# Kernel tuning notes

Hardware: AMD Instinct MI355X
Metric: run time of the kernel (lower is better)

Reference implementation:

```python
import jax, jax.numpy as jnp
import numpy as np

N = 8192      # n_nodes
F = 512       # input feature dim
MLP = 512     # mlp_channels
C = 256       # output channels
H = 2         # MLP layers
KPI = 10      # power iterations
ALPHA = 0.1   # teleport probability


def setup_inputs() -> dict:
    key = jax.random.key(0)
    ks = jax.random.split(key, 10)
    features = jax.random.normal(ks[0], (N, F), dtype=jnp.float32)
    # dense normalized-adjacency surrogate: nonnegative, rows ~ sum to 1
    fltr = jax.random.uniform(ks[1], (N, N), dtype=jnp.float32) * (2.0 / N)
    s = 1.0 / np.sqrt(F)
    W_mlp0 = jax.random.normal(ks[2], (F, MLP), dtype=jnp.float32) * s
    b_mlp0 = jnp.zeros((MLP,), dtype=jnp.float32)
    W_mlp1 = jax.random.normal(ks[3], (MLP, MLP), dtype=jnp.float32) * (1.0 / np.sqrt(MLP))
    b_mlp1 = jnp.zeros((MLP,), dtype=jnp.float32)
    W_out = jax.random.normal(ks[4], (MLP, C), dtype=jnp.float32) * (1.0 / np.sqrt(MLP))
    b_out = jnp.zeros((C,), dtype=jnp.float32)
    return {"features": features, "fltr": fltr,
            "W_mlp0": W_mlp0, "b_mlp0": b_mlp0,
            "W_mlp1": W_mlp1, "b_mlp1": b_mlp1,
            "W_out": W_out, "b_out": b_out}


def reference(features, fltr, W_mlp0, b_mlp0, W_mlp1, b_mlp1, W_out, b_out):
    # MLP stage: per layer -> X = relu( A @ (X W + b) )   (dropout_rate = 0)
    x = features
    for W, b in ((W_mlp0, b_mlp0), (W_mlp1, b_mlp1)):
        x = jnp.matmul(fltr, jnp.matmul(x, W) + b)  # [N, MLP]
        x = jax.nn.relu(x)
    # output projection
    z0 = jnp.matmul(x, W_out) + b_out  # [N, C]
    # K-step APPNP power iteration: Z <- (1-alpha) A Z + alpha Z0
    def step(z, _):
        z = (1.0 - ALPHA) * jnp.matmul(fltr, z) + ALPHA * z0
        return z, None
    z, _ = jax.lax.scan(step, z0, None, length=KPI)
    return jax.nn.softmax(z, axis=-1)
```

## Files before the change

kernel.cpp:

```cpp
#include <hip/hip_runtime.h>

typedef unsigned short u16;
typedef __attribute__((ext_vector_type(8))) short bf16x8;
typedef __attribute__((ext_vector_type(4))) float f32x4;

__device__ __forceinline__ float bf2f(u16 u) {
    union { unsigned i; float f; } v; v.i = ((unsigned)u) << 16; return v.f;
}
__device__ __forceinline__ u16 f2bf(float f) {
    union { float f; unsigned i; } v; v.f = f;
    unsigned r = v.i + 0x7FFFu + ((v.i >> 16) & 1u);
    return (u16)(r >> 16);
}

#define GL2LDS(g, l) __builtin_amdgcn_global_load_lds(                         \
    (const __attribute__((address_space(1))) void*)(g),                        \
    (__attribute__((address_space(3))) void*)(l), 16, 0, 0)

template<int EPI, int AFP32>
__global__ __launch_bounds__(256, 4)
void gemm_bt(const void* __restrict__ Ap, int lda,
             const u16* __restrict__ Bt, int ldb,
             int KB,
             void* __restrict__ outp,
             const void* __restrict__ aux,
             int ldout, int NC)
{
    __shared__ u16 aL[128 * 64];
    __shared__ u16 bL[128 * 64];

    const int t = threadIdx.x;
    const int wid = t >> 6, lane = t & 63;
    const int quad = lane >> 4, l15 = lane & 15, l7 = lane & 7;
    const int m0 = blockIdx.x * 128, n0 = blockIdx.y * 128;
    const int sk = blockIdx.z;
    const int k0 = sk * KB * 64;

    f32x4 acc[4][4];
    const f32x4 z4 = {0.f, 0.f, 0.f, 0.f};
#pragma unroll
    for (int i = 0; i < 4; ++i)
#pragma unroll
        for (int j = 0; j < 4; ++j) acc[i][j] = z4;

    const int wm = (wid >> 1) * 64, wn = (wid & 1) * 64;

    if (AFP32 == 0) {
        const char* pa[4]; const char* pb[4]; int lo[4];
#pragma unroll
        for (int i = 0; i < 4; ++i) {
            int flat = i * 4096 + wid * 1024 + lane * 16;
            int row  = flat >> 7;
            int csrc = ((flat >> 4) & 7) ^ (row & 7);
            pa[i] = (const char*)Ap + ((size_t)(m0 + row) * lda + k0) * 2 + csrc * 16;
            pb[i] = (const char*)Bt + ((size_t)(n0 + row) * ldb + k0) * 2 + csrc * 16;
            lo[i] = i * 4096 + wid * 1024;
        }
        for (int kb = 0; kb < KB; ++kb) {
#pragma unroll
            for (int i = 0; i < 4; ++i) GL2LDS(pa[i], (char*)aL + lo[i]);
#pragma unroll
            for (int i = 0; i < 4; ++i) GL2LDS(pb[i], (char*)bL + lo[i]);
#pragma unroll
            for (int i = 0; i < 4; ++i) { pa[i] += 128; pb[i] += 128; }
            __syncthreads();
#pragma unroll
            for (int ks = 0; ks < 2; ++ks) {
                const int cr = ((ks * 4 + quad) ^ l7) * 8;
                bf16x8 av[4], bv[4];
#pragma unroll
                for (int mi = 0; mi < 4; ++mi)
                    av[mi] = *(const bf16x8*)(aL + (wm + mi * 16 + l15) * 64 + cr);
#pragma unroll
                for (int ni = 0; ni < 4; ++ni)
                    bv[ni] = *(const bf16x8*)(bL + (wn + ni * 16 + l15) * 64 + cr);
#pragma unroll
                for (int mi = 0; mi < 4; ++mi)
#pragma unroll
                    for (int ni = 0; ni < 4; ++ni)
                        acc[mi][ni] = __builtin_amdgcn_mfma_f32_16x16x32_bf16(
                            av[mi], bv[ni], acc[mi][ni], 0, 0, 0);
            }
            __syncthreads();
        }
    } else {
        for (int kb = 0; kb < KB; ++kb) {
            const int kbase = k0 + kb * 64;
#pragma unroll
            for (int i = 0; i < 4; ++i) {
                int flat = i * 4096 + t * 16;
                int row  = flat >> 7;
                int col  = (flat & 127) >> 1;
                bf16x8 v = *(const bf16x8*)(Bt + (size_t)(n0 + row) * ldb + kbase + col);
                *(bf16x8*)(bL + row * 64 + col) = v;
            }
            const float* Af = (const float*)Ap;
#pragma unroll
            for (int j = 0; j < 8; ++j) {
                int f = j * 256 + t;
                int r = f >> 4, c = (f & 15) * 4;
                float4 v = *(const float4*)(Af + (size_t)(m0 + r) * lda + kbase + c);
                ushort4 o;
                o.x = f2bf(v.x); o.y = f2bf(v.y);
                o.z = f2bf(v.z); o.w = f2bf(v.w);
                *(ushort4*)(aL + r * 64 + c) = o;
            }
            __syncthreads();
#pragma unroll
            for (int ks = 0; ks < 2; ++ks) {
                const int cr = (ks * 4 + quad) * 8;
                bf16x8 av[4], bv[4];
#pragma unroll
                for (int mi = 0; mi < 4; ++mi)
                    av[mi] = *(const bf16x8*)(aL + (wm + mi * 16 + l15) * 64 + cr);
#pragma unroll
                for (int ni = 0; ni < 4; ++ni)
                    bv[ni] = *(const bf16x8*)(bL + (wn + ni * 16 + l15) * 64 + cr);
#pragma unroll
                for (int mi = 0; mi < 4; ++mi)
#pragma unroll
                    for (int ni = 0; ni < 4; ++ni)
                        acc[mi][ni] = __builtin_amdgcn_mfma_f32_16x16x32_bf16(
                            av[mi], bv[ni], acc[mi][ni], 0, 0, 0);
            }
            __syncthreads();
        }
    }

    if (EPI == 0) {
#pragma unroll
        for (int ni = 0; ni < 4; ++ni) {
            int n = n0 + wn + ni * 16 + l15;
            float bvv = ((const float*)aux)[n];
            u16* ob = (u16*)outp + (size_t)n * ldout;
#pragma unroll
            for (int mi = 0; mi < 4; ++mi) {
                int m = m0 + wm + mi * 16 + quad * 4;
                ushort4 o;
                o.x = f2bf(acc[mi][ni][0] + bvv);
                o.y = f2bf(acc[mi][ni][1] + bvv);
                o.z = f2bf(acc[mi][ni][2] + bvv);
                o.w = f2bf(acc[mi][ni][3] + bvv);
                *(ushort4*)(ob + m) = o;
            }
        }
    } else if (EPI == 2) {
#pragma unroll
        for (int ni = 0; ni < 4; ++ni) {
            int n = n0 + wn + ni * 16 + l15;
            float* ob = (float*)outp + ((size_t)(sk * NC + n)) * 8192;
#pragma unroll
            for (int mi = 0; mi < 4; ++mi) {
                int m = m0 + wm + mi * 16 + quad * 4;
                float4 o;
                o.x = acc[mi][ni][0]; o.y = acc[mi][ni][1];
                o.z = acc[mi][ni][2]; o.w = acc[mi][ni][3];
                *(float4*)(ob + m) = o;
            }
        }
    } else if (EPI == 3) {
#pragma unroll
        for (int ni = 0; ni < 4; ++ni) {
            int n = n0 + wn + ni * 16 + l15;
            const u16* zrow = (const u16*)aux + (size_t)n * 8192;
            u16* ob = (u16*)outp + (size_t)n * ldout;
#pragma unroll
            for (int mi = 0; mi < 4; ++mi) {
                int m = m0 + wm + mi * 16 + quad * 4;
                ushort4 z0 = *(const ushort4*)(zrow + m);
                ushort4 o;
                o.x = f2bf(0.9f * acc[mi][ni][0] + 0.1f * bf2f(z0.x));
                o.y = f2bf(0.9f * acc[mi][ni][1] + 0.1f * bf2f(z0.y));
                o.z = f2bf(0.9f * acc[mi][ni][2] + 0.1f * bf2f(z0.z));
                o.w = f2bf(0.9f * acc[mi][ni][3] + 0.1f * bf2f(z0.w));
                *(ushort4*)(ob + m) = o;
            }
        }
    } else {
        u16* ob = (u16*)outp;
#pragma unroll
        for (int mi = 0; mi < 4; ++mi) {
            int m = m0 + wm + mi * 16 + quad * 4;
#pragma unroll
            for (int ni = 0; ni < 4; ++ni) {
                int n = n0 + wn + ni * 16 + l15;
#pragma unroll
                for (int r = 0; r < 4; ++r)
                    ob[(size_t)(m + r) * ldout + n] = f2bf(fmaxf(acc[mi][ni][r], 0.0f));
            }
        }
    }
}

__global__ __launch_bounds__(256)
void cvt_f2b_k(const float* __restrict__ in, u16* __restrict__ out, long n4)
{
    long i = (long)blockIdx.x * 256 + threadIdx.x;
    long stride = (long)gridDim.x * 256;
    for (; i < n4; i += stride) {
        float4 v = ((const float4*)in)[i];
        ushort4 o;
        o.x = f2bf(v.x); o.y = f2bf(v.y); o.z = f2bf(v.z); o.w = f2bf(v.w);
        ((ushort4*)out)[i] = o;
    }
}

__global__ __launch_bounds__(256)
void transpose_cvt_k(const float* __restrict__ in, u16* __restrict__ out,
                     int R, int C)
{
    __shared__ u16 tile[32][33];
    int tx = threadIdx.x, ty = threadIdx.y;
    int x = blockIdx.x * 32 + tx;
    int y0 = blockIdx.y * 32 + ty;
#pragma unroll
    for (int j = 0; j < 32; j += 8)
        tile[ty + j][tx] = f2bf(in[(size_t)(y0 + j) * C + x]);
    __syncthreads();
    int x2 = blockIdx.y * 32 + tx;
    int y2 = blockIdx.x * 32 + ty;
#pragma unroll
    for (int j = 0; j < 32; j += 8)
        out[(size_t)(y2 + j) * R + x2] = tile[tx][ty + j];
}

template<int S>
__global__ __launch_bounds__(256)
void combine_bias_k(const float* __restrict__ part, const float* __restrict__ bias,
                    u16* __restrict__ out, long NROW)
{
    const size_t Sz = (size_t)NROW * 8192;
    size_t e = ((size_t)blockIdx.x * 256 + threadIdx.x) * 4;
    int n = (int)(e >> 13);
    float b = bias[n];
    float4 s = *(const float4*)(part + e);
#pragma unroll
    for (int i = 1; i < S; ++i) {
        float4 v = *(const float4*)(part + (size_t)i * Sz + e);
        s.x += v.x; s.y += v.y; s.z += v.z; s.w += v.w;
    }
    ushort4 o;
    o.x = f2bf(s.x + b); o.y = f2bf(s.y + b);
    o.z = f2bf(s.z + b); o.w = f2bf(s.w + b);
    *(ushort4*)(out + e) = o;
}

template<int S>
__global__ __launch_bounds__(256)
void combine_mlp_k(const float* __restrict__ part, u16* __restrict__ y)
{
    __shared__ u16 L[64][68];
    const int t = threadIdx.x;
    const int mb = blockIdx.x * 64;
    const int nb = blockIdx.y * 64;
    const size_t Sz = (size_t)512 * 8192;
#pragma unroll
    for (int i = 0; i < 4; ++i) {
        int flat = i * 256 + t;
        int nl = flat >> 4;
        int mq = flat & 15;
        const float* p0 = part + (size_t)(nb + nl) * 8192 + mb + mq * 4;
        float4 a = *(const float4*)p0;
#pragma unroll
        for (int s = 1; s < S; ++s) {
            float4 v = *(const float4*)(p0 + (size_t)s * Sz);
            a.x += v.x; a.y += v.y; a.z += v.z; a.w += v.w;
        }
        ushort4 o;
        o.x = f2bf(fmaxf(a.x, 0.f)); o.y = f2bf(fmaxf(a.y, 0.f));
        o.z = f2bf(fmaxf(a.z, 0.f)); o.w = f2bf(fmaxf(a.w, 0.f));
        *(ushort4*)&L[nl][mq * 4] = o;
    }
    __syncthreads();
#pragma unroll
    for (int i = 0; i < 4; ++i) {
        int flat = i * 256 + t;
        int ml  = flat >> 4;
        int nl4 = (flat & 15) * 4;
        ushort4 o;
        o.x = L[nl4 + 0][ml]; o.y = L[nl4 + 1][ml];
        o.z = L[nl4 + 2][ml]; o.w = L[nl4 + 3][ml];
        *(ushort4*)(y + (size_t)(mb + ml) * 512 + nb + nl4) = o;
    }
}

template<int S>
__global__ __launch_bounds__(256)
void combine_iter_k(const float* __restrict__ part, const u16* __restrict__ z0T,
                    u16* __restrict__ zT)
{
    const size_t Sz = (size_t)256 * 8192;
    size_t e = ((size_t)blockIdx.x * 256 + threadIdx.x) * 4;
    float4 a = *(const float4*)(part + e);
#pragma unroll
    for (int s = 1; s < S; ++s) {
        float4 v = *(const float4*)(part + (size_t)s * Sz + e);
        a.x += v.x; a.y += v.y; a.z += v.z; a.w += v.w;
    }
    ushort4 z0 = *(const ushort4*)(z0T + e);
    ushort4 o;
    o.x = f2bf(0.9f * a.x + 0.1f * bf2f(z0.x));
    o.y = f2bf(0.9f * a.y + 0.1f * bf2f(z0.y));
    o.z = f2bf(0.9f * a.z + 0.1f * bf2f(z0.z));
    o.w = f2bf(0.9f * a.w + 0.1f * bf2f(z0.w));
    *(ushort4*)(zT + e) = o;
}

__global__ __launch_bounds__(256)
void softmax_k(const u16* __restrict__ zT, float* __restrict__ out)
{
    __shared__ u16 L[64][260];
    const int t = threadIdx.x;
    const int m0 = blockIdx.x * 64;
    const int tx = t & 15, ty = t >> 4;
#pragma unroll
    for (int i = 0; i < 16; ++i) {
        int n = i * 16 + ty;
        ushort4 v = *(const ushort4*)(zT + (size_t)n * 8192 + m0 + tx * 4);
        L[tx * 4 + 0][n] = v.x; L[tx * 4 + 1][n] = v.y;
        L[tx * 4 + 2][n] = v.z; L[tx * 4 + 3][n] = v.w;
    }
    __syncthreads();
    const int wid = t >> 6, lane = t & 63;
    for (int r = 0; r < 16; ++r) {
        int mm = wid * 16 + r;
        ushort4 u = *(const ushort4*)(&L[mm][lane * 4]);
        float f0 = bf2f(u.x), f1 = bf2f(u.y), f2 = bf2f(u.z), f3 = bf2f(u.w);
        float mx = fmaxf(fmaxf(f0, f1), fmaxf(f2, f3));
#pragma unroll
        for (int off = 32; off > 0; off >>= 1) mx = fmaxf(mx, __shfl_xor(mx, off));
        float e0 = __expf(f0 - mx), e1 = __expf(f1 - mx);
        float e2 = __expf(f2 - mx), e3 = __expf(f3 - mx);
        float s = e0 + e1 + e2 + e3;
#pragma unroll
        for (int off = 32; off > 0; off >>= 1) s += __shfl_xor(s, off);
        float inv = 1.0f / s;
        float4 o;
        o.x = e0 * inv; o.y = e1 * inv; o.z = e2 * inv; o.w = e3 * inv;
        *(float4*)(out + (size_t)(m0 + mm) * 256 + lane * 4) = o;
    }
}

extern "C" void kernel_launch(void* const* d_in, const int* in_sizes, int n_in,
                              void* d_out, int out_size, void* d_ws, size_t ws_size,
                              hipStream_t stream)
{
    const float* features = (const float*)d_in[0];
    const float* fltr     = (const float*)d_in[1];
    const float* W0       = (const float*)d_in[2];
    const float* b0       = (const float*)d_in[3];
    const float* W1       = (const float*)d_in[4];
    const float* b1       = (const float*)d_in[5];
    const float* Wo       = (const float*)d_in[6];
    const float* bo       = (const float*)d_in[7];

    dim3 tb(32, 8);

    char* p = (char*)d_ws;
    u16* fB  = (u16*)p;  p += (size_t)8192 * 512 * 2;
    u16* W0T = (u16*)p;  p += (size_t)512 * 512 * 2;
    u16* W1T = (u16*)p;  p += (size_t)512 * 512 * 2;
    u16* WoT = (u16*)p;  p += (size_t)256 * 512 * 2;
    u16* z0T = (u16*)p;  p += (size_t)256 * 8192 * 2;
    u16* zA  = (u16*)p;  p += (size_t)256 * 8192 * 2;
    u16* zB  = (u16*)p;  p += (size_t)256 * 8192 * 2;
    u16* tT  = (u16*)p;  p += (size_t)512 * 8192 * 2;
    u16* y   = (u16*)p;  p += (size_t)8192 * 512 * 2;
    float* part = (float*)p; p += (size_t)4 * 512 * 8192 * 4;
    size_t base_need = (size_t)(p - (char*)d_ws);
    u16* fltrB = (u16*)p;
    size_t full_need = base_need + (size_t)8192 * 8192 * 2;

    if (ws_size >= full_need) {
        cvt_f2b_k<<<2048, 256, 0, stream>>>(fltr, fltrB, (long)8192 * 8192 / 4);
        cvt_f2b_k<<<512, 256, 0, stream>>>(features, fB, (long)8192 * 512 / 4);
        transpose_cvt_k<<<dim3(16, 16), tb, 0, stream>>>(W0, W0T, 512, 512);
        transpose_cvt_k<<<dim3(16, 16), tb, 0, stream>>>(W1, W1T, 512, 512);
        transpose_cvt_k<<<dim3(8, 16),  tb, 0, stream>>>(Wo, WoT, 512, 256);

        gemm_bt<0, 0><<<dim3(64, 4, 1), 256, 0, stream>>>(fB, 512, W0T, 512, 8,
                                                          tT, b0, 8192, 0);
        gemm_bt<2, 0><<<dim3(64, 4, 2), 256, 0, stream>>>(fltrB, 8192, tT, 8192,
                                                          64, part, nullptr, 0, 512);
        combine_mlp_k<2><<<dim3(128, 8), 256, 0, stream>>>(part, y);
        gemm_bt<0, 0><<<dim3(64, 4, 1), 256, 0, stream>>>(y, 512, W1T, 512, 8,
                                                          tT, b1, 8192, 0);
        gemm_bt<2, 0><<<dim3(64, 4, 2), 256, 0, stream>>>(fltrB, 8192, tT, 8192,
                                                          64, part, nullptr, 0, 512);
        combine_mlp_k<2><<<dim3(128, 8), 256, 0, stream>>>(part, y);
        gemm_bt<0, 0><<<dim3(64, 2, 1), 256, 0, stream>>>(y, 512, WoT, 512, 8,
                                                          z0T, bo, 8192, 0);
        const u16* src = z0T;
        for (int it = 0; it < 10; ++it) {
            u16* dst = (it & 1) ? zB : zA;
            gemm_bt<2, 0><<<dim3(64, 2, 4), 256, 0, stream>>>(fltrB, 8192, src,
                                                              8192, 32, part,
                                                              nullptr, 0, 256);
            combine_iter_k<4><<<2048, 256, 0, stream>>>(part, z0T, dst);
            src = dst;
        }
        softmax_k<<<128, 256, 0, stream>>>(src, (float*)d_out);
    } else if (ws_size >= base_need) {
        cvt_f2b_k<<<512, 256, 0, stream>>>(features, fB, (long)8192 * 512 / 4);
        transpose_cvt_k<<<dim3(16, 16), tb, 0, stream>>>(W0, W0T, 512, 512);
        transpose_cvt_k<<<dim3(16, 16), tb, 0, stream>>>(W1, W1T, 512, 512);
        transpose_cvt_k<<<dim3(8, 16),  tb, 0, stream>>>(Wo, WoT, 512, 256);

        gemm_bt<2, 0><<<dim3(64, 4, 2), 256, 0, stream>>>(fB, 512, W0T, 512, 4,
                                                          part, nullptr, 0, 512);
        combine_bias_k<2><<<4096, 256, 0, stream>>>(part, b0, tT, 512);
        gemm_bt<2, 1><<<dim3(64, 4, 4), 256, 0, stream>>>(fltr, 8192, tT, 8192,
                                                          32, part, nullptr, 0, 512);
        combine_mlp_k<4><<<dim3(128, 8), 256, 0, stream>>>(part, y);
        gemm_bt<2, 0><<<dim3(64, 4, 2), 256, 0, stream>>>(y, 512, W1T, 512, 4,
                                                          part, nullptr, 0, 512);
        combine_bias_k<2><<<4096, 256, 0, stream>>>(part, b1, tT, 512);
        gemm_bt<2, 1><<<dim3(64, 4, 4), 256, 0, stream>>>(fltr, 8192, tT, 8192,
                                                          32, part, nullptr, 0, 512);
        combine_mlp_k<4><<<dim3(128, 8), 256, 0, stream>>>(part, y);
        gemm_bt<2, 0><<<dim3(64, 2, 4), 256, 0, stream>>>(y, 512, WoT, 512, 2,
                                                          part, nullptr, 0, 256);
        combine_bias_k<4><<<2048, 256, 0, stream>>>(part, bo, z0T, 256);
        const u16* src = z0T;
        for (int it = 0; it < 10; ++it) {
            u16* dst = (it & 1) ? zB : zA;
            gemm_bt<2, 1><<<dim3(64, 2, 8), 256, 0, stream>>>(fltr, 8192, src,
                                                              8192, 16, part,
                                                              nullptr, 0, 256);
            combine_iter_k<8><<<2048, 256, 0, stream>>>(part, z0T, dst);
            src = dst;
        }
        softmax_k<<<128, 256, 0, stream>>>(src, (float*)d_out);
    } else {
        char* w = (char*)d_ws;
        u16* fW0T = (u16*)w;  w += (size_t)512 * 512 * 2;
        u16* fW1T = (u16*)w;  w += (size_t)512 * 512 * 2;
        u16* fWoT = (u16*)w;  w += (size_t)256 * 512 * 2;
        u16* fz0T = (u16*)w;  w += (size_t)256 * 8192 * 2;
        char* rb = w;
        u16* ftT = (u16*)rb;
        u16* fy  = (u16*)(rb + (size_t)512 * 8192 * 2);
        u16* fzA = (u16*)rb;
        u16* fzB = (u16*)(rb + (size_t)256 * 8192 * 2);

        transpose_cvt_k<<<dim3(16, 16), tb, 0, stream>>>(W0, fW0T, 512, 512);
        transpose_cvt_k<<<dim3(16, 16), tb, 0, stream>>>(W1, fW1T, 512, 512);
        transpose_cvt_k<<<dim3(8, 16),  tb, 0, stream>>>(Wo, fWoT, 512, 256);
        gemm_bt<0, 1><<<dim3(64, 4), 256, 0, stream>>>(features, 512, fW0T, 512, 8,
                                                       ftT, b0, 8192, 0);
        gemm_bt<1, 1><<<dim3(64, 4), 256, 0, stream>>>(fltr, 8192, ftT, 8192, 128,
                                                       fy, nullptr, 512, 0);
        gemm_bt<0, 0><<<dim3(64, 4), 256, 0, stream>>>(fy, 512, fW1T, 512, 8,
                                                       ftT, b1, 8192, 0);
        gemm_bt<1, 1><<<dim3(64, 4), 256, 0, stream>>>(fltr, 8192, ftT, 8192, 128,
                                                       fy, nullptr, 512, 0);
        gemm_bt<0, 0><<<dim3(64, 2), 256, 0, stream>>>(fy, 512, fWoT, 512, 8,
                                                       fz0T, bo, 8192, 0);
        const u16* src = fz0T;
        for (int it = 0; it < 10; ++it) {
            u16* dst = (it & 1) ? fzB : fzA;
            gemm_bt<3, 1><<<dim3(64, 2), 256, 0, stream>>>(fltr, 8192, src, 8192,
                                                           128, dst, fz0T, 8192, 0);
            src = dst;
        }
        softmax_k<<<128, 256, 0, stream>>>(src, (float*)d_out);
    }
}
```

Measured before the change: 1.142 ms.

## Fuse split-K reduction into power-iteration GEMM via atomic last-block combine

Replaces the separate combine_iter_k launch after each split-K power-iteration GEMM with an in-kernel reduction. Each split writes its fp32 partials, bumps an atomic tile counter, and the last-arriving block sums the other splits' partials and applies the APPNP update epilogue. This removes ten extra kernel launches and the full partial re-read pass. The cost is a fence, an atomic per tile and serialized epilogue work in one block per tile. Correctness relies on the counter being zeroed once and using modulo across iterations.

```diff
diff --git a/kernel.cpp b/kernel.cpp
--- a/kernel.cpp
+++ b/kernel.cpp
@@ -17,17 +17,20 @@
     (const __attribute__((address_space(1))) void*)(g),                        \
     (__attribute__((address_space(3))) void*)(l), 16, 0, 0)
 
-template<int EPI, int AFP32>
+template<int EPI, int AFP32, int SK>
 __global__ __launch_bounds__(256, 4)
 void gemm_bt(const void* __restrict__ Ap, int lda,
              const u16* __restrict__ Bt, int ldb,
              int KB,
              void* __restrict__ outp,
              const void* __restrict__ aux,
-             int ldout, int NC)
+             int ldout, int NC,
+             float* __restrict__ part,
+             unsigned* __restrict__ ctr)
 {
     __shared__ u16 aL[128 * 64];
     __shared__ u16 bL[128 * 64];
+    __shared__ int lastFlag;
 
     const int t = threadIdx.x;
     const int wid = t >> 6, lane = t & 63;
@@ -176,6 +179,55 @@
                 *(ushort4*)(ob + m) = o;
             }
         }
+    } else if (EPI == 4) {
+#pragma unroll
+        for (int ni = 0; ni < 4; ++ni) {
+            int n = n0 + wn + ni * 16 + l15;
+            float* ob = part + ((size_t)(sk * NC + n)) * 8192;
+#pragma unroll
+            for (int mi = 0; mi < 4; ++mi) {
+                int m = m0 + wm + mi * 16 + quad * 4;
+                float4 o;
+                o.x = acc[mi][ni][0]; o.y = acc[mi][ni][1];
+                o.z = acc[mi][ni][2]; o.w = acc[mi][ni][3];
+                *(float4*)(ob + m) = o;
+            }
+        }
+        __threadfence();
+        if (t == 0) {
+            unsigned old = atomicAdd(&ctr[blockIdx.x * gridDim.y + blockIdx.y], 1u);
+            lastFlag = (((old + 1) % (unsigned)SK) == 0u) ? 1 : 0;
+        }
+        __syncthreads();
+        if (lastFlag) {
+            __threadfence();
+#pragma unroll
+            for (int ni = 0; ni < 4; ++ni) {
+                int n = n0 + wn + ni * 16 + l15;
+                const u16* zrow = (const u16*)aux + (size_t)n * 8192;
+                u16* ob = (u16*)outp + (size_t)n * ldout;
+#pragma unroll
+                for (int mi = 0; mi < 4; ++mi) {
+                    int m = m0 + wm + mi * 16 + quad * 4;
+                    float sx = acc[mi][ni][0], sy = acc[mi][ni][1];
+                    float sz = acc[mi][ni][2], sw = acc[mi][ni][3];
+#pragma unroll
+                    for (int s = 0; s < SK; ++s) {
+                        if (s == sk) continue;
+                        float4 v = *(const float4*)(part +
+                                     ((size_t)(s * NC + n)) * 8192 + m);
+                        sx += v.x; sy += v.y; sz += v.z; sw += v.w;
+                    }
+                    ushort4 z0 = *(const ushort4*)(zrow + m);
+                    ushort4 o;
+                    o.x = f2bf(0.9f * sx + 0.1f * bf2f(z0.x));
+                    o.y = f2bf(0.9f * sy + 0.1f * bf2f(z0.y));
+                    o.z = f2bf(0.9f * sz + 0.1f * bf2f(z0.z));
+                    o.w = f2bf(0.9f * sw + 0.1f * bf2f(z0.w));
+                    *(ushort4*)(ob + m) = o;
+                }
+            }
+        }
     } else {
         u16* ob = (u16*)outp;
 #pragma unroll
@@ -190,6 +242,13 @@
             }
         }
     }
+}
+
+__global__ __launch_bounds__(256)
+void zero_ctr_k(unsigned* __restrict__ c, int n)
+{
+    int i = blockIdx.x * 256 + threadIdx.x;
+    if (i < n) c[i] = 0u;
 }
 
 __global__ __launch_bounds__(256)
@@ -367,6 +426,7 @@
     u16* tT  = (u16*)p;  p += (size_t)512 * 8192 * 2;
     u16* y   = (u16*)p;  p += (size_t)8192 * 512 * 2;
     float* part = (float*)p; p += (size_t)4 * 512 * 8192 * 4;
+    unsigned* ctr = (unsigned*)p; p += 1024;
     size_t base_need = (size_t)(p - (char*)d_ws);
     u16* fltrB = (u16*)p;
     size_t full_need = base_need + (size_t)8192 * 8192 * 2;
@@ -377,26 +437,32 @@
         transpose_cvt_k<<<dim3(16, 16), tb, 0, stream>>>(W0, W0T, 512, 512);
         transpose_cvt_k<<<dim3(16, 16), tb, 0, stream>>>(W1, W1T, 512, 512);
         transpose_cvt_k<<<dim3(8, 16),  tb, 0, stream>>>(Wo, WoT, 512, 256);
-
-        gemm_bt<0, 0><<<dim3(64, 4, 1), 256, 0, stream>>>(fB, 512, W0T, 512, 8,
-                                                          tT, b0, 8192, 0);
-        gemm_bt<2, 0><<<dim3(64, 4, 2), 256, 0, stream>>>(fltrB, 8192, tT, 8192,
-                                                          64, part, nullptr, 0, 512);
+        zero_ctr_k<<<1, 256, 0, stream>>>(ctr, 256);
+
+        gemm_bt<0, 0, 1><<<dim3(64, 4, 1), 256, 0, stream>>>(fB, 512, W0T, 512, 8,
+                                                          tT, b0, 8192, 0,
+                                                          nullptr, nullptr);
+        gemm_bt<2, 0, 1><<<dim3(64, 4, 2), 256, 0, stream>>>(fltrB, 8192, tT, 8192,
+                                                          64, part, nullptr, 0, 512,
+                                                          nullptr, nullptr);
         combine_mlp_k<2><<<dim3(128, 8), 256, 0, stream>>>(part, y);
-        gemm_bt<0, 0><<<dim3(64, 4, 1), 256, 0, stream>>>(y, 512, W1T, 512, 8,
-                                                          tT, b1, 8192, 0);
-        gemm_bt<2, 0><<<dim3(64, 4, 2), 256, 0, stream>>>(fltrB, 8192, tT, 8192,
-                                                          64, part, nullptr, 0, 512);
+        gemm_bt<0, 0, 1><<<dim3(64, 4, 1), 256, 0, stream>>>(y, 512, W1T, 512, 8,
+                                                          tT, b1, 8192, 0,
+                                                          nullptr, nullptr);
+        gemm_bt<2, 0, 1><<<dim3(64, 4, 2), 256, 0, stream>>>(fltrB, 8192, tT, 8192,
+                                                          64, part, nullptr, 0, 512,
+                                                          nullptr, nullptr);
         combine_mlp_k<2><<<dim3(128, 8), 256, 0, stream>>>(part, y);
-        gemm_bt<0, 0><<<dim3(64, 2, 1), 256, 0, stream>>>(y, 512, WoT, 512, 8,
-                                                          z0T, bo, 8192, 0);
+        gemm_bt<0, 0, 1><<<dim3(64, 2, 1), 256, 0, stream>>>(y, 512, WoT, 512, 8,
+                                                          z0T, bo, 8192, 0,
+                                                          nullptr, nullptr);
         const u16* src = z0T;
         for (int it = 0; it < 10; ++it) {
             u16* dst = (it & 1) ? zB : zA;
-            gemm_bt<2, 0><<<dim3(64, 2, 4), 256, 0, stream>>>(fltrB, 8192, src,
-                                                              8192, 32, part,
-                                                              nullptr, 0, 256);
-            combine_iter_k<4><<<2048, 256, 0, stream>>>(part, z0T, dst);
+            gemm_bt<4, 0, 4><<<dim3(64, 2, 4), 256, 0, stream>>>(fltrB, 8192, src,
+                                                              8192, 32, dst,
+                                                              z0T, 8192, 256,
+                                                              part, ctr);
             src = dst;
         }
         softmax_k<<<128, 256, 0, stream>>>(src, (float*)d_out);
@@ -406,27 +472,33 @@
         transpose_cvt_k<<<dim3(16, 16), tb, 0, stream>>>(W1, W1T, 512, 512);
         transpose_cvt_k<<<dim3(8, 16),  tb, 0, stream>>>(Wo, WoT, 512, 256);
 
-        gemm_bt<2, 0><<<dim3(64, 4, 2), 256, 0, stream>>>(fB, 512, W0T, 512, 4,
-                                                          part, nullptr, 0, 512);
+        gemm_bt<2, 0, 1><<<dim3(64, 4, 2), 256, 0, stream>>>(fB, 512, W0T, 512, 4,
+                                                          part, nullptr, 0, 512,
+                                                          nullptr, nullptr);
         combine_bias_k<2><<<4096, 256, 0, stream>>>(part, b0, tT, 512);
-        gemm_bt<2, 1><<<dim3(64, 4, 4), 256, 0, stream>>>(fltr, 8192, tT, 8192,
-                                                          32, part, nullptr, 0, 512);
+        gemm_bt<2, 1, 1><<<dim3(64, 4, 4), 256, 0, stream>>>(fltr, 8192, tT, 8192,
+                                                          32, part, nullptr, 0, 512,
+                                                          nullptr, nullptr);
         combine_mlp_k<4><<<dim3(128, 8), 256, 0, stream>>>(part, y);
-        gemm_bt<2, 0><<<dim3(64, 4, 2), 256, 0, stream>>>(y, 512, W1T, 512, 4,
-                                                          part, nullptr, 0, 512);
+        gemm_bt<2, 0, 1><<<dim3(64, 4, 2), 256, 0, stream>>>(y, 512, W1T, 512, 4,
+                                                          part, nullptr, 0, 512,
+                                                          nullptr, nullptr);
         combine_bias_k<2><<<4096, 256, 0, stream>>>(part, b1, tT, 512);
-        gemm_bt<2, 1><<<dim3(64, 4, 4), 256, 0, stream>>>(fltr, 8192, tT, 8192,
-                                                          32, part, nullptr, 0, 512);
+        gemm_bt<2, 1, 1><<<dim3(64, 4, 4), 256, 0, stream>>>(fltr, 8192, tT, 8192,
+                                                          32, part, nullptr, 0, 512,
+                                                          nullptr, nullptr);
         combine_mlp_k<4><<<dim3(128, 8), 256, 0, stream>>>(part, y);
-        gemm_bt<2, 0><<<dim3(64, 2, 4), 256, 0, stream>>>(y, 512, WoT, 512, 2,
-                                                          part, nullptr, 0, 256);
+        gemm_bt<2, 0, 1><<<dim3(64, 2, 4), 256, 0, stream>>>(y, 512, WoT, 512, 2,
+                                                          part, nullptr, 0, 256,
+                                                          nullptr, nullptr);
         combine_bias_k<4><<<2048, 256, 0, stream>>>(part, bo, z0T, 256);
         const u16* src = z0T;
         for (int it = 0; it < 10; ++it) {
             u16* dst = (it & 1) ? zB : zA;
-            gemm_bt<2, 1><<<dim3(64, 2, 8), 256, 0, stream>>>(fltr, 8192, src,
+            gemm_bt<2, 1, 1><<<dim3(64, 2, 8), 256, 0, stream>>>(fltr, 8192, src,
                                                               8192, 16, part,
-                                                              nullptr, 0, 256);
+                                                              nullptr, 0, 256,
+                                                              nullptr, nullptr);
             combine_iter_k<8><<<2048, 256, 0, stream>>>(part, z0T, dst);
             src = dst;
         }
@@ -446,21 +518,27 @@
         transpose_cvt_k<<<dim3(16, 16), tb, 0, stream>>>(W0, fW0T, 512, 512);
         transpose_cvt_k<<<dim3(16, 16), tb, 0, stream>>>(W1, fW1T, 512, 512);
         transpose_cvt_k<<<dim3(8, 16),  tb, 0, stream>>>(Wo, fWoT, 512, 256);
-        gemm_bt<0, 1><<<dim3(64, 4), 256, 0, stream>>>(features, 512, fW0T, 512, 8,
-                                                       ftT, b0, 8192, 0);
-        gemm_bt<1, 1><<<dim3(64, 4), 256, 0, stream>>>(fltr, 8192, ftT, 8192, 128,
-                                                       fy, nullptr, 512, 0);
-        gemm_bt<0, 0><<<dim3(64, 4), 256, 0, stream>>>(fy, 512, fW1T, 512, 8,
-                                                       ftT, b1, 8192, 0);
-        gemm_bt<1, 1><<<dim3(64, 4), 256, 0, stream>>>(fltr, 8192, ftT, 8192, 128,
-                                                       fy, nullptr, 512, 0);
-        gemm_bt<0, 0><<<dim3(64, 2), 256, 0, stream>>>(fy, 512, fWoT, 512, 8,
-                                                       fz0T, bo, 8192, 0);
+        gemm_bt<0, 1, 1><<<dim3(64, 4), 256, 0, stream>>>(features, 512, fW0T, 512, 8,
+                                                       ftT, b0, 8192, 0,
+                                                       nullptr, nullptr);
+        gemm_bt<1, 1, 1><<<dim3(64, 4), 256, 0, stream>>>(fltr, 8192, ftT, 8192, 128,
+                                                       fy, nullptr, 512, 0,
+                                                       nullptr, nullptr);
+        gemm_bt<0, 0, 1><<<dim3(64, 4), 256, 0, stream>>>(fy, 512, fW1T, 512, 8,
+                                                       ftT, b1, 8192, 0,
+                                                       nullptr, nullptr);
+        gemm_bt<1, 1, 1><<<dim3(64, 4), 256, 0, stream>>>(fltr, 8192, ftT, 8192, 128,
+                                                       fy, nullptr, 512, 0,
+                                                       nullptr, nullptr);
+        gemm_bt<0, 0, 1><<<dim3(64, 2), 256, 0, stream>>>(fy, 512, fWoT, 512, 8,
+                                                       fz0T, bo, 8192, 0,
+                                                       nullptr, nullptr);
         const u16* src = fz0T;
         for (int it = 0; it < 10; ++it) {
             u16* dst = (it & 1) ? fzB : fzA;
-            gemm_bt<3, 1><<<dim3(64, 2), 256, 0, stream>>>(fltr, 8192, src, 8192,
-                                                           128, dst, fz0T, 8192, 0);
+            gemm_bt<3, 1, 1><<<dim3(64, 2), 256, 0, stream>>>(fltr, 8192, src, 8192,
+                                                           128, dst, fz0T, 8192, 0,
+                                                           nullptr, nullptr);
             src = dst;
         }
         softmax_k<<<128, 256, 0, stream>>>(src, (float*)d_out);
```

Measured after the change: 1.924 ms. 68.5% more time.
